# Kernel tuning notes

Measured on AMD Instinct MI355X. Metric: run time of the kernel, lower is better.

The kernel has to match this reference:

```python
import jax, jax.numpy as jnp
import numpy as np

DK, DL, HID = 128, 128, 128  # per init_kwargs: mlp_list=[256,128,128]


def setup_inputs() -> dict:
    key = jax.random.key(0)
    k1, k2, k3, k4, k5 = jax.random.split(key, 5)
    B, K, L = 2, 128, 4096
    inputA = jax.random.normal(k1, (B, K, DK), dtype=jnp.float32)
    inputB = jax.random.normal(k2, (B, L, DL), dtype=jnp.float32)
    # MLP layer 0: Linear(256 -> 128), kaiming-uniform-ish init
    lim1 = 1.0 / np.sqrt(DK + DL)
    W1 = jax.random.uniform(k3, (DK + DL, HID), jnp.float32, -lim1, lim1)
    b1 = jax.random.uniform(k4, (HID,), jnp.float32, -lim1, lim1)
    # scoring Linear(128 -> 1, bias=False)
    lim2 = 1.0 / np.sqrt(HID)
    w2 = jax.random.uniform(k5, (HID,), jnp.float32, -lim2, lim2)
    return {"inputA": inputA, "inputB": inputB, "W1": W1, "b1": b1,
            "w2": w2, "nA": K, "nB": L}


def reference(inputA, inputB, W1, b1, w2, nA, nB):
    # Original: tC = cat([repeat(A), repeat(B)], -1); mlp(tC); linear; softmax(L).
    # Fused-equivalent math: split W1 rows between the A-part and B-part of the
    # concat, so the first Linear is two small matmuls + broadcast add.
    hA = jnp.einsum('bkd,dh->bkh', inputA, W1[:DK])        # (B, K, H)
    hB = jnp.einsum('bld,dh->blh', inputB, W1[DK:])        # (B, L, H)
    h = jax.nn.relu(hA[:, :, None, :] + hB[:, None, :, :] + b1)  # (B, K, L, H)
    scores = jnp.einsum('bklh,h->bkl', h, w2)              # (B, K, L)
    return jax.nn.softmax(scores, axis=2)
```

## Files before the change

### kernel.cpp

```cpp
#include <hip/hip_runtime.h>
#include <hip/hip_fp16.h>
#include <math.h>

constexpr int BB = 2;
constexpr int KK = 128;
constexpr int LL = 4096;
constexpr int DD = 128;
constexpr int HH = 128;

__device__ __forceinline__ float4 ld4(const float* p) {
    return *reinterpret_cast<const float4*>(p);
}

__device__ __forceinline__ __half2 hmax2(__half2 a, __half2 b) {
    unsigned ua = __builtin_bit_cast(unsigned, a);
    unsigned ub = __builtin_bit_cast(unsigned, b);
    unsigned ud;
    asm("v_pk_max_f16 %0, %1, %2" : "=v"(ud) : "v"(ua), "v"(ub));
    return __builtin_bit_cast(__half2, ud);
}

__device__ __forceinline__ uint32_t duph(float x) {
    __half h = __float2half(x);
    unsigned short us = __builtin_bit_cast(unsigned short, h);
    return (uint32_t)us * 0x10001u;
}

__global__ __launch_bounds__(256) void k1_gemm(
    const float* __restrict__ inA, const float* __restrict__ inB,
    const float* __restrict__ W1, const float* __restrict__ b1,
    const float* __restrict__ w2,
    uint32_t* __restrict__ u_dup, uint32_t* __restrict__ w2_dup,
    __half* __restrict__ vT)
{
    __shared__ __align__(16) float sIn[16 * 128];
    __shared__ float sT[128 * 17];

    const int j = blockIdx.x;
    const bool isA = (j >= 512);
    int row0;
    if (isA) {
        row0 = (j - 512) * 16;
    } else {
        const int C = j & 15, s = j >> 4;
        row0 = (C * 32 + s) * 16;
    }
    const float* src = isA ? (inA + (size_t)row0 * DD)
                           : (inB + (size_t)row0 * DD);
    const float* w   = W1 + (isA ? 0 : DD * HH);

    const int tid = threadIdx.x;

    #pragma unroll
    for (int q = 0; q < 2; ++q) {
        const int idx = tid + 256 * q;
        reinterpret_cast<float4*>(sIn)[idx] =
            reinterpret_cast<const float4*>(src)[idx];
    }
    __syncthreads();

    const int tx = tid & 31;
    const int ty = tid >> 5;

    float acc[2][4];
    #pragma unroll
    for (int r = 0; r < 2; ++r)
        #pragma unroll
        for (int c = 0; c < 4; ++c) acc[r][c] = 0.f;

    for (int d0 = 0; d0 < DD; d0 += 4) {
        float4 w4[4];
        #pragma unroll
        for (int dd = 0; dd < 4; ++dd)
            w4[dd] = ld4(&w[(size_t)(d0 + dd) * HH + tx * 4]);
        float a[2][4];
        #pragma unroll
        for (int r = 0; r < 2; ++r) {
            float4 a4 = ld4(&sIn[(ty * 2 + r) * 128 + d0]);
            a[r][0] = a4.x; a[r][1] = a4.y; a[r][2] = a4.z; a[r][3] = a4.w;
        }
        #pragma unroll
        for (int dd = 0; dd < 4; ++dd) {
            #pragma unroll
            for (int r = 0; r < 2; ++r) {
                const float av = a[r][dd];
                acc[r][0] = fmaf(av, w4[dd].x, acc[r][0]);
                acc[r][1] = fmaf(av, w4[dd].y, acc[r][1]);
                acc[r][2] = fmaf(av, w4[dd].z, acc[r][2]);
                acc[r][3] = fmaf(av, w4[dd].w, acc[r][3]);
            }
        }
    }

    if (isA) {
        const float4 bb = ld4(&b1[tx * 4]);
        #pragma unroll
        for (int r = 0; r < 2; ++r) {
            uint4 o;
            o.x = duph(acc[r][0] + bb.x);
            o.y = duph(acc[r][1] + bb.y);
            o.z = duph(acc[r][2] + bb.z);
            o.w = duph(acc[r][3] + bb.w);
            *reinterpret_cast<uint4*>(
                &u_dup[(size_t)(row0 + ty * 2 + r) * HH + tx * 4]) = o;
        }
        if (j == 512 && tid < HH) w2_dup[tid] = duph(w2[tid]);
    } else {
        #pragma unroll
        for (int r = 0; r < 2; ++r) {
            const int l = ty * 2 + r;
            sT[(tx * 4 + 0) * 17 + l] = acc[r][0];
            sT[(tx * 4 + 1) * 17 + l] = acc[r][1];
            sT[(tx * 4 + 2) * 17 + l] = acc[r][2];
            sT[(tx * 4 + 3) * 17 + l] = acc[r][3];
        }
        __syncthreads();
        const int h    = tid >> 1;
        const int half = tid & 1;
        const int bsel = row0 >> 12;
        const int l0g  = (row0 & 4095) + half * 8;
        uint4 o;
        uint32_t* op = reinterpret_cast<uint32_t*>(&o);
        #pragma unroll
        for (int i = 0; i < 4; ++i) {
            const float lo = sT[h * 17 + half * 8 + 2 * i];
            const float hi = sT[h * 17 + half * 8 + 2 * i + 1];
            op[i] = __builtin_bit_cast(uint32_t, __floats2half2_rn(lo, hi));
        }
        uint32_t* dst = reinterpret_cast<uint32_t*>(vT) +
                        (size_t)(bsel * HH + h) * (LL / 2) + l0g / 2;
        *reinterpret_cast<uint4*>(dst) = o;
    }
}

__global__ __launch_bounds__(256) void k2_score(
    const uint32_t* __restrict__ u_dup, const uint32_t* __restrict__ w2_dup,
    const __half* __restrict__ vT, float* __restrict__ out)
{
    __shared__ __align__(16) uint32_t sU[4 * HH];
    __shared__ __align__(16) uint32_t sW[HH];

    int m = blockIdx.x;
    const int cb = m & 7;   m >>= 3;
    const int kt = m & 31;  m >>= 5;
    const int b  = m;
    const int tid = threadIdx.x;

    if (tid < 128)
        reinterpret_cast<uint4*>(sU)[tid] =
            reinterpret_cast<const uint4*>(u_dup + (size_t)(b * KK + kt * 4) * HH)[tid];
    else if (tid < 160)
        reinterpret_cast<uint4*>(sW)[tid - 128] =
            reinterpret_cast<const uint4*>(w2_dup)[tid - 128];
    __syncthreads();

    const int p = cb * 256 + tid;
    const uint32_t* vp = reinterpret_cast<const uint32_t*>(vT)
                         + (size_t)b * HH * (LL / 2) + p;

    const __half2 hz = __float2half2_rn(0.f);
    float2 facc[4];
    #pragma unroll
    for (int k = 0; k < 4; ++k) { facc[k].x = 0.f; facc[k].y = 0.f; }

    for (int g = 0; g < 8; ++g) {
        const int h0 = g * 16;
        uint32_t v[16];
        #pragma unroll
        for (int jj = 0; jj < 16; ++jj)
            v[jj] = vp[(size_t)(h0 + jj) * (LL / 2)];

        __half2 acc[4];
        #pragma unroll
        for (int k = 0; k < 4; ++k) acc[k] = hz;

        #pragma unroll
        for (int k = 0; k < 4; ++k) {
            #pragma unroll
            for (int q = 0; q < 4; ++q) {
                const uint4 uc = *reinterpret_cast<const uint4*>(&sU[k * HH + h0 + q * 4]);
                const uint4 wc = *reinterpret_cast<const uint4*>(&sW[h0 + q * 4]);
                const uint32_t* uq = reinterpret_cast<const uint32_t*>(&uc);
                const uint32_t* wq = reinterpret_cast<const uint32_t*>(&wc);
                #pragma unroll
                for (int jj = 0; jj < 4; ++jj) {
                    const __half2 uu = __builtin_bit_cast(__half2, uq[jj]);
                    const __half2 ww = __builtin_bit_cast(__half2, wq[jj]);
                    __half2 t = __hadd2(__builtin_bit_cast(__half2, v[q * 4 + jj]), uu);
                    acc[k] = __hfma2(hmax2(t, hz), ww, acc[k]);
                }
            }
        }
        #pragma unroll
        for (int k = 0; k < 4; ++k) {
            const float2 f = __half22float2(acc[k]);
            facc[k].x += f.x; facc[k].y += f.y;
        }
    }

    #pragma unroll
    for (int k = 0; k < 4; ++k)
        *reinterpret_cast<float2*>(
            &out[(size_t)(b * KK + kt * 4 + k) * LL + 2 * p]) = facc[k];
}

__global__ __launch_bounds__(1024) void k3_softmax(float* __restrict__ out)
{
    __shared__ float redm[16];
    __shared__ float reds[16];

    const int row = blockIdx.x;
    float* p = out + (size_t)row * LL;
    const int tid = threadIdx.x;

    float4 x = reinterpret_cast<const float4*>(p)[tid];

    float m = fmaxf(fmaxf(x.x, x.y), fmaxf(x.z, x.w));
    #pragma unroll
    for (int off = 32; off > 0; off >>= 1)
        m = fmaxf(m, __shfl_xor(m, off, 64));
    const int lane = tid & 63, wv = tid >> 6;
    if (lane == 0) redm[wv] = m;
    __syncthreads();
    if (tid < 16) {
        float mm = redm[tid];
        #pragma unroll
        for (int off = 8; off > 0; off >>= 1)
            mm = fmaxf(mm, __shfl_xor(mm, off, 64));
        redm[tid] = mm;
    }
    __syncthreads();
    m = redm[0];

    x.x = expf(x.x - m); x.y = expf(x.y - m);
    x.z = expf(x.z - m); x.w = expf(x.w - m);
    float s = (x.x + x.y) + (x.z + x.w);
    #pragma unroll
    for (int off = 32; off > 0; off >>= 1)
        s += __shfl_xor(s, off, 64);
    if (lane == 0) reds[wv] = s;
    __syncthreads();
    if (tid < 16) {
        float ss = reds[tid];
        #pragma unroll
        for (int off = 8; off > 0; off >>= 1)
            ss += __shfl_xor(ss, off, 64);
        reds[tid] = ss;
    }
    __syncthreads();
    s = reds[0];

    const float inv = 1.0f / s;
    x.x *= inv; x.y *= inv; x.z *= inv; x.w *= inv;
    reinterpret_cast<float4*>(p)[tid] = x;
}

extern "C" void kernel_launch(void* const* d_in, const int* in_sizes, int n_in,
                              void* d_out, int out_size, void* d_ws, size_t ws_size,
                              hipStream_t stream)
{
    const float* inA = (const float*)d_in[0];
    const float* inB = (const float*)d_in[1];
    const float* W1  = (const float*)d_in[2];
    const float* b1  = (const float*)d_in[3];
    const float* w2  = (const float*)d_in[4];
    float* out = (float*)d_out;

    uint32_t* u_dup  = (uint32_t*)d_ws;
    uint32_t* w2_dup = (uint32_t*)((char*)d_ws + 128 * 1024);
    __half*   vT     = (__half*)((char*)d_ws + 128 * 1024 + 512);

    hipLaunchKernelGGL(k1_gemm, dim3(528), dim3(256), 0, stream,
                       inA, inB, W1, b1, w2, u_dup, w2_dup, vT);
    hipLaunchKernelGGL(k2_score, dim3(512), dim3(256), 0, stream,
                       u_dup, w2_dup, vT, out);
    hipLaunchKernelGGL(k3_softmax, dim3(BB * KK), dim3(1024), 0, stream, out);
}
```

Measured before the change: 33.95 us.

## Stage W1 in shared memory, double rows per block, and reorder score loop

The GEMM kernel now processes 32 rows per block instead of 16, halving the grid, and stages the W1 weight matrix in shared memory in two halves rather than reading it from global memory per thread. This is meant to cut redundant global weight loads and raise arithmetic per block. The block-to-row mapping for the B input changes, and the transposed fp16 writeback now stores 32 columns per row. The score kernel's inner loop is reordered so each v and w value is loaded once and reused across the four k rows. The larger shared-memory footprint (49KB) and fewer blocks may lower occupancy.

```diff
diff --git a/kernel.cpp b/kernel.cpp
--- a/kernel.cpp
+++ b/kernel.cpp
@@ -33,61 +33,73 @@
     uint32_t* __restrict__ u_dup, uint32_t* __restrict__ w2_dup,
     __half* __restrict__ vT)
 {
-    __shared__ __align__(16) float sIn[16 * 128];
-    __shared__ float sT[128 * 17];
-
-    const int j = blockIdx.x;
-    const bool isA = (j >= 512);
+    __shared__ __align__(16) char smem[49 * 1024];
+    float*  sIn = reinterpret_cast<float*>(smem);
+    float4* sW4 = reinterpret_cast<float4*>(smem + 16 * 1024);
+    float*  sT  = reinterpret_cast<float*>(smem + 16 * 1024);
+
+    const int bid = blockIdx.x;
+    const int tid = threadIdx.x;
+
     int row0;
-    if (isA) {
-        row0 = (j - 512) * 16;
+    bool isA;
+    if (bid < 256) {
+        const int x = bid & 7, y = bid >> 3;
+        const int C = x + 8 * (y & 1);
+        row0 = C * 512 + (y >> 1) * 32;
+        isA = false;
     } else {
-        const int C = j & 15, s = j >> 4;
-        row0 = (C * 32 + s) * 16;
-    }
-    const float* src = isA ? (inA + (size_t)row0 * DD)
-                           : (inB + (size_t)row0 * DD);
-    const float* w   = W1 + (isA ? 0 : DD * HH);
-
-    const int tid = threadIdx.x;
-
-    #pragma unroll
-    for (int q = 0; q < 2; ++q) {
-        const int idx = tid + 256 * q;
+        row0 = (bid - 256) * 32;
+        isA = true;
+    }
+    const float* src = (isA ? inA : inB) + (size_t)row0 * DD;
+    const float4* wsrc = reinterpret_cast<const float4*>(W1 + (isA ? 0 : DD * HH));
+
+    #pragma unroll
+    for (int j = 0; j < 4; ++j) {
+        const int idx = tid + 256 * j;
         reinterpret_cast<float4*>(sIn)[idx] =
             reinterpret_cast<const float4*>(src)[idx];
     }
-    __syncthreads();
 
     const int tx = tid & 31;
     const int ty = tid >> 5;
 
-    float acc[2][4];
-    #pragma unroll
-    for (int r = 0; r < 2; ++r)
-        #pragma unroll
-        for (int c = 0; c < 4; ++c) acc[r][c] = 0.f;
-
-    for (int d0 = 0; d0 < DD; d0 += 4) {
-        float4 w4[4];
-        #pragma unroll
-        for (int dd = 0; dd < 4; ++dd)
-            w4[dd] = ld4(&w[(size_t)(d0 + dd) * HH + tx * 4]);
-        float a[2][4];
-        #pragma unroll
-        for (int r = 0; r < 2; ++r) {
-            float4 a4 = ld4(&sIn[(ty * 2 + r) * 128 + d0]);
-            a[r][0] = a4.x; a[r][1] = a4.y; a[r][2] = a4.z; a[r][3] = a4.w;
-        }
-        #pragma unroll
-        for (int dd = 0; dd < 4; ++dd) {
-            #pragma unroll
-            for (int r = 0; r < 2; ++r) {
-                const float av = a[r][dd];
-                acc[r][0] = fmaf(av, w4[dd].x, acc[r][0]);
-                acc[r][1] = fmaf(av, w4[dd].y, acc[r][1]);
-                acc[r][2] = fmaf(av, w4[dd].z, acc[r][2]);
-                acc[r][3] = fmaf(av, w4[dd].w, acc[r][3]);
+    float accx[4], accy[4], accz[4], accw[4];
+    #pragma unroll
+    for (int r = 0; r < 4; ++r) { accx[r] = accy[r] = accz[r] = accw[r] = 0.f; }
+
+    for (int wh = 0; wh < 2; ++wh) {
+        __syncthreads();
+        #pragma unroll
+        for (int q = 0; q < 8; ++q)
+            sW4[tid + 256 * q] = wsrc[wh * 2048 + tid + 256 * q];
+        __syncthreads();
+
+        #pragma unroll 2
+        for (int dd0 = 0; dd0 < 64; dd0 += 4) {
+            const int d0 = wh * 64 + dd0;
+            float4 w4[4];
+            #pragma unroll
+            for (int dd = 0; dd < 4; ++dd)
+                w4[dd] = sW4[(dd0 + dd) * 32 + tx];
+            float a[4][4];
+            #pragma unroll
+            for (int r = 0; r < 4; ++r) {
+                float4 a4 = ld4(&sIn[(ty * 4 + r) * 128 + d0]);
+                a[r][0] = a4.x; a[r][1] = a4.y; a[r][2] = a4.z; a[r][3] = a4.w;
+            }
+            #pragma unroll
+            for (int dd = 0; dd < 4; ++dd) {
+                const float4 wv = w4[dd];
+                #pragma unroll
+                for (int r = 0; r < 4; ++r) {
+                    const float av = a[r][dd];
+                    accx[r] = fmaf(av, wv.x, accx[r]);
+                    accy[r] = fmaf(av, wv.y, accy[r]);
+                    accz[r] = fmaf(av, wv.z, accz[r]);
+                    accw[r] = fmaf(av, wv.w, accw[r]);
+                }
             }
         }
     }
@@ -95,41 +107,44 @@
     if (isA) {
         const float4 bb = ld4(&b1[tx * 4]);
         #pragma unroll
-        for (int r = 0; r < 2; ++r) {
+        for (int r = 0; r < 4; ++r) {
             uint4 o;
-            o.x = duph(acc[r][0] + bb.x);
-            o.y = duph(acc[r][1] + bb.y);
-            o.z = duph(acc[r][2] + bb.z);
-            o.w = duph(acc[r][3] + bb.w);
+            o.x = duph(accx[r] + bb.x);
+            o.y = duph(accy[r] + bb.y);
+            o.z = duph(accz[r] + bb.z);
+            o.w = duph(accw[r] + bb.w);
             *reinterpret_cast<uint4*>(
-                &u_dup[(size_t)(row0 + ty * 2 + r) * HH + tx * 4]) = o;
-        }
-        if (j == 512 && tid < HH) w2_dup[tid] = duph(w2[tid]);
+                &u_dup[(size_t)(row0 + ty * 4 + r) * HH + tx * 4]) = o;
+        }
+        if (bid == 256 && tid < HH) w2_dup[tid] = duph(w2[tid]);
     } else {
-        #pragma unroll
-        for (int r = 0; r < 2; ++r) {
-            const int l = ty * 2 + r;
-            sT[(tx * 4 + 0) * 17 + l] = acc[r][0];
-            sT[(tx * 4 + 1) * 17 + l] = acc[r][1];
-            sT[(tx * 4 + 2) * 17 + l] = acc[r][2];
-            sT[(tx * 4 + 3) * 17 + l] = acc[r][3];
+        __syncthreads();
+        #pragma unroll
+        for (int r = 0; r < 4; ++r) {
+            const int l = ty * 4 + r;
+            sT[(tx * 4 + 0) * 33 + l] = accx[r];
+            sT[(tx * 4 + 1) * 33 + l] = accy[r];
+            sT[(tx * 4 + 2) * 33 + l] = accz[r];
+            sT[(tx * 4 + 3) * 33 + l] = accw[r];
         }
         __syncthreads();
         const int h    = tid >> 1;
         const int half = tid & 1;
         const int bsel = row0 >> 12;
-        const int l0g  = (row0 & 4095) + half * 8;
-        uint4 o;
-        uint32_t* op = reinterpret_cast<uint32_t*>(&o);
-        #pragma unroll
-        for (int i = 0; i < 4; ++i) {
-            const float lo = sT[h * 17 + half * 8 + 2 * i];
-            const float hi = sT[h * 17 + half * 8 + 2 * i + 1];
-            op[i] = __builtin_bit_cast(uint32_t, __floats2half2_rn(lo, hi));
+        const int l0   = (row0 & 4095) + half * 16;
+        uint32_t o[8];
+        #pragma unroll
+        for (int i = 0; i < 8; ++i) {
+            const float lo = sT[h * 33 + half * 16 + 2 * i];
+            const float hi = sT[h * 33 + half * 16 + 2 * i + 1];
+            o[i] = __builtin_bit_cast(uint32_t, __floats2half2_rn(lo, hi));
         }
         uint32_t* dst = reinterpret_cast<uint32_t*>(vT) +
-                        (size_t)(bsel * HH + h) * (LL / 2) + l0g / 2;
-        *reinterpret_cast<uint4*>(dst) = o;
+                        (size_t)(bsel * HH + h) * (LL / 2) + l0 / 2;
+        uint4 s0; s0.x = o[0]; s0.y = o[1]; s0.z = o[2]; s0.w = o[3];
+        uint4 s1; s1.x = o[4]; s1.y = o[5]; s1.z = o[6]; s1.w = o[7];
+        *reinterpret_cast<uint4*>(dst)     = s0;
+        *reinterpret_cast<uint4*>(dst + 4) = s1;
     }
 }
 
@@ -175,18 +190,21 @@
         for (int k = 0; k < 4; ++k) acc[k] = hz;
 
         #pragma unroll
-        for (int k = 0; k < 4; ++k) {
-            #pragma unroll
-            for (int q = 0; q < 4; ++q) {
-                const uint4 uc = *reinterpret_cast<const uint4*>(&sU[k * HH + h0 + q * 4]);
-                const uint4 wc = *reinterpret_cast<const uint4*>(&sW[h0 + q * 4]);
-                const uint32_t* uq = reinterpret_cast<const uint32_t*>(&uc);
-                const uint32_t* wq = reinterpret_cast<const uint32_t*>(&wc);
+        for (int q = 0; q < 4; ++q) {
+            const uint4 wc = *reinterpret_cast<const uint4*>(&sW[h0 + q * 4]);
+            uint4 uc[4];
+            #pragma unroll
+            for (int k = 0; k < 4; ++k)
+                uc[k] = *reinterpret_cast<const uint4*>(&sU[k * HH + h0 + q * 4]);
+            const uint32_t* wq = reinterpret_cast<const uint32_t*>(&wc);
+            #pragma unroll
+            for (int jj = 0; jj < 4; ++jj) {
+                const __half2 ww = __builtin_bit_cast(__half2, wq[jj]);
+                const __half2 vv = __builtin_bit_cast(__half2, v[q * 4 + jj]);
                 #pragma unroll
-                for (int jj = 0; jj < 4; ++jj) {
-                    const __half2 uu = __builtin_bit_cast(__half2, uq[jj]);
-                    const __half2 ww = __builtin_bit_cast(__half2, wq[jj]);
-                    __half2 t = __hadd2(__builtin_bit_cast(__half2, v[q * 4 + jj]), uu);
+                for (int k = 0; k < 4; ++k) {
+                    const uint32_t* uq = reinterpret_cast<const uint32_t*>(&uc[k]);
+                    __half2 t = __hadd2(vv, __builtin_bit_cast(__half2, uq[jj]));
                     acc[k] = __hfma2(hmax2(t, hz), ww, acc[k]);
                 }
             }
@@ -266,11 +284,12 @@
     const float* w2  = (const float*)d_in[4];
     float* out = (float*)d_out;
 
-    uint32_t* u_dup  = (uint32_t*)d_ws;
-    uint32_t* w2_dup = (uint32_t*)((char*)d_ws + 128 * 1024);
-    __half*   vT     = (__half*)((char*)d_ws + 128 * 1024 + 512);
-
-    hipLaunchKernelGGL(k1_gemm, dim3(528), dim3(256), 0, stream,
+    char* ws = (char*)d_ws;
+    uint32_t* u_dup  = (uint32_t*)ws;
+    uint32_t* w2_dup = (uint32_t*)(ws + 0x20000);
+    __half*   vT     = (__half*)(ws + 0x40000);
+
+    hipLaunchKernelGGL(k1_gemm, dim3(264), dim3(256), 0, stream,
                        inA, inB, W1, b1, w2, u_dup, w2_dup, vT);
     hipLaunchKernelGGL(k2_score, dim3(512), dim3(256), 0, stream,
                        u_dup, w2_dup, vT, out);
```

Result: faster. 30.68 us (-9.6%).
